# Kernel tuning notes

Measured on AMD Instinct MI355X. Metric: run time of the kernel, lower is better.

The kernel has to match this reference:

```python
import jax, jax.numpy as jnp
import numpy as np

N = 65536
NUM_STATE = 128
NUM_HIDDEN = 256
NUM_EMBED = 128


def setup_inputs() -> dict:
    key = jax.random.key(0)
    ks = jax.random.split(key, 8)
    s1 = jax.random.normal(ks[0], (N, NUM_STATE), dtype=jnp.float32)
    s2 = jax.random.normal(ks[1], (N, NUM_STATE), dtype=jnp.float32)
    # kaiming_normal_(fan_in, linear): std = 1/sqrt(fan_in)
    W1 = jax.random.normal(ks[2], (NUM_HIDDEN, NUM_STATE), dtype=jnp.float32) / np.sqrt(NUM_STATE)
    b1 = jnp.zeros((NUM_HIDDEN,), dtype=jnp.float32)
    W2 = jax.random.normal(ks[3], (NUM_HIDDEN, NUM_HIDDEN), dtype=jnp.float32) / np.sqrt(NUM_HIDDEN)
    b2 = jnp.zeros((NUM_HIDDEN,), dtype=jnp.float32)
    W3 = jax.random.normal(ks[4], (NUM_EMBED, NUM_HIDDEN), dtype=jnp.float32) / np.sqrt(NUM_HIDDEN)
    b3 = jnp.zeros((NUM_EMBED,), dtype=jnp.float32)
    return {"s1": s1, "s2": s2, "W1": W1, "b1": b1, "W2": W2, "b2": b2, "W3": W3, "b3": b3}


def _embed(x, W1, b1, W2, b2, W3, b3):
    h = jax.nn.selu(x @ W1.T + b1)
    h = jax.nn.selu(h @ W2.T + b2)
    return h @ W3.T + b3  # [N, num_embedding]


def reference(s1, s2, W1, b1, W2, b2, W3, b3):
    e1 = _embed(s1, W1, b1, W2, b2, W3, b3)
    e2 = _embed(s2, W1, b1, W2, b2, W3, b3)
    # diag(e1 @ e2.T) == per-row dot product (same math, O(N*d) not O(N^2*d))
    dots = jnp.einsum('nd,nd->n', e1, e2)
    out = dots / (jnp.linalg.norm(e1, axis=1) * jnp.linalg.norm(e2, axis=1))
    out = (out + 1.0) / 2.0
    return jax.nn.sigmoid(out)
```

## Files before the change

### kernel.cpp

```cpp
#include <hip/hip_runtime.h>


typedef __bf16 bf16x8 __attribute__((ext_vector_type(8)));
typedef __bf16 bf16x4 __attribute__((ext_vector_type(4)));
typedef float  f32x4  __attribute__((ext_vector_type(4)));

constexpr int WS_W1 = 0;
constexpr int WS_W2 = 32768;
constexpr int WS_W3 = 98304;

__device__ __forceinline__ float selu_f(float x) {
    const float scale = 1.0507009873554805f;
    const float sa    = 1.7580993408473766f;
    float xp = fmaxf(x, 0.f);
    float xn = fminf(x, 0.f);
    return fmaf(scale, xp, sa * (__expf(xn) - 1.f));
}

__device__ __forceinline__ bf16x8 read_act(const __bf16* lds, int row, int kcol) {
    unsigned byte = (unsigned)((row * 128 + kcol) * 2) ^ ((unsigned)(row & 7) << 4);
    return *(const bf16x8*)((const char*)lds + byte);
}

template<bool SELU>
__device__ __forceinline__ void store_act(__bf16* lds, int row, int col0, f32x4 a) {
    float v0 = a[0], v1 = a[1], v2 = a[2], v3 = a[3];
    if (SELU) { v0 = selu_f(v0); v1 = selu_f(v1); v2 = selu_f(v2); v3 = selu_f(v3); }
    bf16x4 u;
    u[0] = (__bf16)v0; u[1] = (__bf16)v1; u[2] = (__bf16)v2; u[3] = (__bf16)v3;
    unsigned byte = (unsigned)((row * 128 + col0) * 2) ^ ((unsigned)(row & 7) << 4);
    *(bf16x4*)((char*)lds + byte) = u;
}

__global__ void pack_weights_kernel(const float* __restrict__ W1,
                                    const float* __restrict__ W2,
                                    const float* __restrict__ W3,
                                    __bf16* __restrict__ ws) {
    int t = blockIdx.x * blockDim.x + threadIdx.x;
    const float* W; int K, KS, f, base;
    if (t < 4096)       { W = W1; K = 128; KS = 4; f = t;         base = WS_W1; }
    else if (t < 12288) { W = W2; K = 256; KS = 8; f = t - 4096;  base = WS_W2; }
    else                { W = W3; K = 256; KS = 8; f = t - 12288; base = WS_W3; }
    int lane = f & 63;
    int ks   = (f >> 6) % KS;
    int ct   = f / (64 * KS);
    int row  = ct * 16 + (lane & 15);
    int k0   = ks * 32 + (lane >> 4) * 8;
    const float* src = W + (size_t)row * K + k0;
    __bf16* dst = ws + base + (size_t)f * 8;
#pragma unroll
    for (int j = 0; j < 8; ++j) dst[j] = (__bf16)src[j];
}

__global__ __launch_bounds__(512, 4)
void embed_sim_kernel(const float* __restrict__ s1, const float* __restrict__ s2,
                      const float* __restrict__ b1, const float* __restrict__ b2,
                      const float* __restrict__ b3,
                      const __bf16* __restrict__ wf, float* __restrict__ out) {
    __shared__ __align__(16) __bf16 Xs[64 * 128];
    __shared__ __align__(16) __bf16 hA[64 * 128];
    __shared__ __align__(16) __bf16 hB[64 * 128];

    const int tid  = threadIdx.x;
    const int wave = tid >> 6;
    const int lane = tid & 63;
    const int lr   = lane & 15;
    const int kg   = lane >> 4;
    const int p0   = blockIdx.x * 32;

#pragma unroll
    for (int it = 0; it < 2; ++it) {
        int idx = tid + it * 512;
        int row = idx >> 4;
        int k0  = (idx & 15) << 3;
        const float* src = (row < 32) ? (s1 + (size_t)(p0 + row) * 128 + k0)
                                      : (s2 + (size_t)(p0 + row - 32) * 128 + k0);
        float4 v0 = *(const float4*)(src);
        float4 v1 = *(const float4*)(src + 4);
        bf16x8 w;
        w[0] = (__bf16)v0.x; w[1] = (__bf16)v0.y; w[2] = (__bf16)v0.z; w[3] = (__bf16)v0.w;
        w[4] = (__bf16)v1.x; w[5] = (__bf16)v1.y; w[6] = (__bf16)v1.z; w[7] = (__bf16)v1.w;
        unsigned byte = (unsigned)((row * 128 + k0) * 2) ^ ((unsigned)(row & 7) << 4);
        *(bf16x8*)((char*)Xs + byte) = w;
    }
    __syncthreads();

    {
        bf16x8 wfr[2][4]; f32x4 bv[2];
#pragma unroll
        for (int ti = 0; ti < 2; ++ti) {
            int t = wave * 2 + ti;
#pragma unroll
            for (int ks = 0; ks < 4; ++ks)
                wfr[ti][ks] = *(const bf16x8*)(wf + WS_W1 + (size_t)((t * 4 + ks) * 64 + lane) * 8);
            bv[ti] = *(const f32x4*)(b1 + t * 16 + kg * 4);
        }
#pragma unroll
        for (int s = 0; s < 4; ++s) {
            bf16x8 xfr[4];
#pragma unroll
            for (int ks = 0; ks < 4; ++ks) xfr[ks] = read_act(Xs, s * 16 + lr, ks * 32 + kg * 8);
#pragma unroll
            for (int ti = 0; ti < 2; ++ti) {
                f32x4 acc = bv[ti];
#pragma unroll
                for (int ks = 0; ks < 4; ++ks)
                    acc = __builtin_amdgcn_mfma_f32_16x16x32_bf16(wfr[ti][ks], xfr[ks], acc, 0, 0, 0);
                int t = wave * 2 + ti;
                store_act<true>((t < 8) ? hA : hB, s * 16 + lr, (t & 7) * 16 + kg * 4, acc);
            }
        }
    }
    __syncthreads();

    {
        f32x4 acc[2][4];
        bf16x8 wfr[2][8];
#pragma unroll
        for (int ti = 0; ti < 2; ++ti) {
            int t = wave * 2 + ti;
#pragma unroll
            for (int ks = 0; ks < 8; ++ks)
                wfr[ti][ks] = *(const bf16x8*)(wf + WS_W2 + (size_t)((t * 8 + ks) * 64 + lane) * 8);
            f32x4 b = *(const f32x4*)(b2 + t * 16 + kg * 4);
#pragma unroll
            for (int s = 0; s < 4; ++s) acc[ti][s] = b;
        }
#pragma unroll
        for (int s = 0; s < 4; ++s) {
            const int row = s * 16 + lr;
            bf16x8 hfr[8];
#pragma unroll
            for (int ks = 0; ks < 4; ++ks) {
                hfr[ks]     = read_act(hA, row, ks * 32 + kg * 8);
                hfr[4 + ks] = read_act(hB, row, ks * 32 + kg * 8);
            }
#pragma unroll
            for (int ti = 0; ti < 2; ++ti)
#pragma unroll
                for (int ks = 0; ks < 8; ++ks)
                    acc[ti][s] = __builtin_amdgcn_mfma_f32_16x16x32_bf16(
                        wfr[ti][ks], hfr[ks], acc[ti][s], 0, 0, 0);
        }
        if (wave < 4) {
#pragma unroll
            for (int ti = 0; ti < 2; ++ti)
#pragma unroll
                for (int s = 0; s < 4; ++s)
                    store_act<true>(Xs, s * 16 + lr, (wave * 2 + ti) * 16 + kg * 4, acc[ti][s]);
        }
        __syncthreads();
        if (wave >= 4) {
#pragma unroll
            for (int ti = 0; ti < 2; ++ti)
#pragma unroll
                for (int s = 0; s < 4; ++s)
                    store_act<true>(hA, s * 16 + lr, ((wave - 4) * 2 + ti) * 16 + kg * 4, acc[ti][s]);
        }
    }
    __syncthreads();

    {
        bf16x8 wfr[8]; f32x4 bv;
        const int t = wave;
#pragma unroll
        for (int ks = 0; ks < 8; ++ks)
            wfr[ks] = *(const bf16x8*)(wf + WS_W3 + (size_t)((t * 8 + ks) * 64 + lane) * 8);
        bv = *(const f32x4*)(b3 + t * 16 + kg * 4);
#pragma unroll
        for (int s = 0; s < 4; ++s) {
            const int row = s * 16 + lr;
            bf16x8 hfr[8];
#pragma unroll
            for (int ks = 0; ks < 4; ++ks) {
                hfr[ks]     = read_act(Xs, row, ks * 32 + kg * 8);
                hfr[4 + ks] = read_act(hA, row, ks * 32 + kg * 8);
            }
            f32x4 acc = bv;
#pragma unroll
            for (int ks = 0; ks < 8; ++ks)
                acc = __builtin_amdgcn_mfma_f32_16x16x32_bf16(wfr[ks], hfr[ks], acc, 0, 0, 0);
            store_act<false>(hB, row, t * 16 + kg * 4, acc);
        }
    }
    __syncthreads();

    const int p  = tid >> 4;
    const int dg = tid & 15;
    const int d0 = dg * 8;
    float dot = 0.f, n1 = 0.f, n2 = 0.f;
    {
        unsigned by1 = (unsigned)((p * 128 + d0) * 2) ^ ((unsigned)(p & 7) << 4);
        unsigned by2 = (unsigned)(((p + 32) * 128 + d0) * 2) ^ ((unsigned)((p + 32) & 7) << 4);
        bf16x8 e1 = *(const bf16x8*)((const char*)hB + by1);
        bf16x8 e2 = *(const bf16x8*)((const char*)hB + by2);
#pragma unroll
        for (int j = 0; j < 8; ++j) {
            float a = (float)e1[j], b = (float)e2[j];
            dot = fmaf(a, b, dot);
            n1  = fmaf(a, a, n1);
            n2  = fmaf(b, b, n2);
        }
    }
#pragma unroll
    for (int off = 1; off < 16; off <<= 1) {
        dot += __shfl_xor(dot, off);
        n1  += __shfl_xor(n1,  off);
        n2  += __shfl_xor(n2,  off);
    }
    if (dg == 0) {
        float r = dot * rsqrtf(n1 * n2);
        float x = (r + 1.f) * 0.5f;
        out[p0 + p] = 1.f / (1.f + __expf(-x));
    }
}

extern "C" void kernel_launch(void* const* d_in, const int* in_sizes, int n_in,
                              void* d_out, int out_size, void* d_ws, size_t ws_size,
                              hipStream_t stream) {
    const float* s1 = (const float*)d_in[0];
    const float* s2 = (const float*)d_in[1];
    const float* W1 = (const float*)d_in[2];
    const float* b1 = (const float*)d_in[3];
    const float* W2 = (const float*)d_in[4];
    const float* b2 = (const float*)d_in[5];
    const float* W3 = (const float*)d_in[6];
    const float* b3 = (const float*)d_in[7];
    __bf16* wf = (__bf16*)d_ws;
    float*  outp = (float*)d_out;

    pack_weights_kernel<<<64, 256, 0, stream>>>(W1, W2, W3, wf);

    const int npairs = in_sizes[0] / 128;
    embed_sim_kernel<<<npairs / 32, 512, 0, stream>>>(s1, s2, b1, b2, b3, wf, outp);
}
```

Measured before the change: 61.01 us.

## Halve block to 256 threads with more output tiles per wave

The fused embedding kernel now runs 4 waves per block instead of 8. Each wave computes twice as many output column tiles, and the layer-2 and layer-3 weights are loaded in two K halves to limit register pressure. The LDS layout moves from three 64x128 buffers to one 64x128 buffer plus one 64x256 buffer that is reused for the final embeddings. The aim is more MFMA work per wave and amortised activation fragment reads, in exchange for more accumulators per thread and changed occupancy limits (launch bounds 256,3).

After: 58.22 us. -4.6%, faster.

```diff
diff --git a/kernel.cpp b/kernel.cpp
--- a/kernel.cpp
+++ b/kernel.cpp
@@ -17,18 +17,19 @@
     return fmaf(scale, xp, sa * (__expf(xn) - 1.f));
 }
 
+template<int COLS>
 __device__ __forceinline__ bf16x8 read_act(const __bf16* lds, int row, int kcol) {
-    unsigned byte = (unsigned)((row * 128 + kcol) * 2) ^ ((unsigned)(row & 7) << 4);
+    unsigned byte = (unsigned)((row * COLS + kcol) * 2) ^ ((unsigned)(row & 7) << 4);
     return *(const bf16x8*)((const char*)lds + byte);
 }
 
-template<bool SELU>
+template<bool SELU, int COLS>
 __device__ __forceinline__ void store_act(__bf16* lds, int row, int col0, f32x4 a) {
     float v0 = a[0], v1 = a[1], v2 = a[2], v3 = a[3];
     if (SELU) { v0 = selu_f(v0); v1 = selu_f(v1); v2 = selu_f(v2); v3 = selu_f(v3); }
     bf16x4 u;
     u[0] = (__bf16)v0; u[1] = (__bf16)v1; u[2] = (__bf16)v2; u[3] = (__bf16)v3;
-    unsigned byte = (unsigned)((row * 128 + col0) * 2) ^ ((unsigned)(row & 7) << 4);
+    unsigned byte = (unsigned)((row * COLS + col0) * 2) ^ ((unsigned)(row & 7) << 4);
     *(bf16x4*)((char*)lds + byte) = u;
 }
 
@@ -52,14 +53,13 @@
     for (int j = 0; j < 8; ++j) dst[j] = (__bf16)src[j];
 }
 
-__global__ __launch_bounds__(512, 4)
+__global__ __launch_bounds__(256, 3)
 void embed_sim_kernel(const float* __restrict__ s1, const float* __restrict__ s2,
                       const float* __restrict__ b1, const float* __restrict__ b2,
                       const float* __restrict__ b3,
                       const __bf16* __restrict__ wf, float* __restrict__ out) {
     __shared__ __align__(16) __bf16 Xs[64 * 128];
-    __shared__ __align__(16) __bf16 hA[64 * 128];
-    __shared__ __align__(16) __bf16 hB[64 * 128];
+    __shared__ __align__(16) __bf16 hA[64 * 256];
 
     const int tid  = threadIdx.x;
     const int wave = tid >> 6;
@@ -68,9 +68,12 @@
     const int kg   = lane >> 4;
     const int p0   = blockIdx.x * 32;
 
-#pragma unroll
-    for (int it = 0; it < 2; ++it) {
-        int idx = tid + it * 512;
+    __bf16* h2hi = hA;
+    __bf16* Es   = hA + 64 * 128;
+
+#pragma unroll
+    for (int it = 0; it < 4; ++it) {
+        int idx = tid + it * 256;
         int row = idx >> 4;
         int k0  = (idx & 15) << 3;
         const float* src = (row < 32) ? (s1 + (size_t)(p0 + row) * 128 + k0)
@@ -86,10 +89,10 @@
     __syncthreads();
 
     {
-        bf16x8 wfr[2][4]; f32x4 bv[2];
-#pragma unroll
-        for (int ti = 0; ti < 2; ++ti) {
-            int t = wave * 2 + ti;
+        bf16x8 wfr[4][4]; f32x4 bv[4];
+#pragma unroll
+        for (int ti = 0; ti < 4; ++ti) {
+            int t = wave * 4 + ti;
 #pragma unroll
             for (int ks = 0; ks < 4; ++ks)
                 wfr[ti][ks] = *(const bf16x8*)(wf + WS_W1 + (size_t)((t * 4 + ks) * 64 + lane) * 8);
@@ -97,103 +100,125 @@
         }
 #pragma unroll
         for (int s = 0; s < 4; ++s) {
+            const int row = s * 16 + lr;
             bf16x8 xfr[4];
 #pragma unroll
-            for (int ks = 0; ks < 4; ++ks) xfr[ks] = read_act(Xs, s * 16 + lr, ks * 32 + kg * 8);
-#pragma unroll
-            for (int ti = 0; ti < 2; ++ti) {
+            for (int ks = 0; ks < 4; ++ks) xfr[ks] = read_act<128>(Xs, row, ks * 32 + kg * 8);
+#pragma unroll
+            for (int ti = 0; ti < 4; ++ti) {
                 f32x4 acc = bv[ti];
 #pragma unroll
                 for (int ks = 0; ks < 4; ++ks)
                     acc = __builtin_amdgcn_mfma_f32_16x16x32_bf16(wfr[ti][ks], xfr[ks], acc, 0, 0, 0);
-                int t = wave * 2 + ti;
-                store_act<true>((t < 8) ? hA : hB, s * 16 + lr, (t & 7) * 16 + kg * 4, acc);
-            }
+                store_act<true, 256>(hA, row, (wave * 4 + ti) * 16 + kg * 4, acc);
+            }
+        }
+    }
+    __syncthreads();
+
+    {
+        f32x4 acc[4][4];
+#pragma unroll
+        for (int ti = 0; ti < 4; ++ti) {
+            f32x4 b = *(const f32x4*)(b2 + (wave * 4 + ti) * 16 + kg * 4);
+#pragma unroll
+            for (int s = 0; s < 4; ++s) acc[ti][s] = b;
+        }
+#pragma unroll
+        for (int kh = 0; kh < 2; ++kh) {
+            bf16x8 wfr[4][4];
+#pragma unroll
+            for (int ti = 0; ti < 4; ++ti) {
+                int t = wave * 4 + ti;
+#pragma unroll
+                for (int ks = 0; ks < 4; ++ks)
+                    wfr[ti][ks] = *(const bf16x8*)(wf + WS_W2 + (size_t)((t * 8 + kh * 4 + ks) * 64 + lane) * 8);
+            }
+#pragma unroll
+            for (int s = 0; s < 4; ++s) {
+                const int row = s * 16 + lr;
+                bf16x8 hfr[4];
+#pragma unroll
+                for (int ks = 0; ks < 4; ++ks)
+                    hfr[ks] = read_act<256>(hA, row, kh * 128 + ks * 32 + kg * 8);
+#pragma unroll
+                for (int ti = 0; ti < 4; ++ti)
+#pragma unroll
+                    for (int ks = 0; ks < 4; ++ks)
+                        acc[ti][s] = __builtin_amdgcn_mfma_f32_16x16x32_bf16(
+                            wfr[ti][ks], hfr[ks], acc[ti][s], 0, 0, 0);
+            }
+        }
+        if (wave < 2) {
+#pragma unroll
+            for (int ti = 0; ti < 4; ++ti)
+#pragma unroll
+                for (int s = 0; s < 4; ++s)
+                    store_act<true, 128>(Xs, s * 16 + lr, (wave * 4 + ti) * 16 + kg * 4, acc[ti][s]);
+        }
+        __syncthreads();
+        if (wave >= 2) {
+#pragma unroll
+            for (int ti = 0; ti < 4; ++ti)
+#pragma unroll
+                for (int s = 0; s < 4; ++s)
+                    store_act<true, 128>(h2hi, s * 16 + lr, ((wave - 2) * 4 + ti) * 16 + kg * 4, acc[ti][s]);
         }
     }
     __syncthreads();
 
     {
         f32x4 acc[2][4];
-        bf16x8 wfr[2][8];
 #pragma unroll
         for (int ti = 0; ti < 2; ++ti) {
-            int t = wave * 2 + ti;
-#pragma unroll
-            for (int ks = 0; ks < 8; ++ks)
-                wfr[ti][ks] = *(const bf16x8*)(wf + WS_W2 + (size_t)((t * 8 + ks) * 64 + lane) * 8);
-            f32x4 b = *(const f32x4*)(b2 + t * 16 + kg * 4);
+            f32x4 b = *(const f32x4*)(b3 + (wave * 2 + ti) * 16 + kg * 4);
 #pragma unroll
             for (int s = 0; s < 4; ++s) acc[ti][s] = b;
         }
 #pragma unroll
-        for (int s = 0; s < 4; ++s) {
-            const int row = s * 16 + lr;
-            bf16x8 hfr[8];
-#pragma unroll
-            for (int ks = 0; ks < 4; ++ks) {
-                hfr[ks]     = read_act(hA, row, ks * 32 + kg * 8);
-                hfr[4 + ks] = read_act(hB, row, ks * 32 + kg * 8);
-            }
-#pragma unroll
-            for (int ti = 0; ti < 2; ++ti)
-#pragma unroll
-                for (int ks = 0; ks < 8; ++ks)
-                    acc[ti][s] = __builtin_amdgcn_mfma_f32_16x16x32_bf16(
-                        wfr[ti][ks], hfr[ks], acc[ti][s], 0, 0, 0);
-        }
-        if (wave < 4) {
-#pragma unroll
-            for (int ti = 0; ti < 2; ++ti)
-#pragma unroll
-                for (int s = 0; s < 4; ++s)
-                    store_act<true>(Xs, s * 16 + lr, (wave * 2 + ti) * 16 + kg * 4, acc[ti][s]);
-        }
-        __syncthreads();
-        if (wave >= 4) {
-#pragma unroll
-            for (int ti = 0; ti < 2; ++ti)
-#pragma unroll
-                for (int s = 0; s < 4; ++s)
-                    store_act<true>(hA, s * 16 + lr, ((wave - 4) * 2 + ti) * 16 + kg * 4, acc[ti][s]);
-        }
-    }
-    __syncthreads();
-
-    {
-        bf16x8 wfr[8]; f32x4 bv;
-        const int t = wave;
-#pragma unroll
-        for (int ks = 0; ks < 8; ++ks)
-            wfr[ks] = *(const bf16x8*)(wf + WS_W3 + (size_t)((t * 8 + ks) * 64 + lane) * 8);
-        bv = *(const f32x4*)(b3 + t * 16 + kg * 4);
-#pragma unroll
-        for (int s = 0; s < 4; ++s) {
-            const int row = s * 16 + lr;
-            bf16x8 hfr[8];
-#pragma unroll
-            for (int ks = 0; ks < 4; ++ks) {
-                hfr[ks]     = read_act(Xs, row, ks * 32 + kg * 8);
-                hfr[4 + ks] = read_act(hA, row, ks * 32 + kg * 8);
-            }
-            f32x4 acc = bv;
-#pragma unroll
-            for (int ks = 0; ks < 8; ++ks)
-                acc = __builtin_amdgcn_mfma_f32_16x16x32_bf16(wfr[ks], hfr[ks], acc, 0, 0, 0);
-            store_act<false>(hB, row, t * 16 + kg * 4, acc);
-        }
-    }
-    __syncthreads();
-
-    const int p  = tid >> 4;
-    const int dg = tid & 15;
-    const int d0 = dg * 8;
+        for (int kh = 0; kh < 2; ++kh) {
+            const __bf16* src = (kh == 0) ? Xs : h2hi;
+            bf16x8 wfr[2][4];
+#pragma unroll
+            for (int ti = 0; ti < 2; ++ti) {
+                int t = wave * 2 + ti;
+#pragma unroll
+                for (int ks = 0; ks < 4; ++ks)
+                    wfr[ti][ks] = *(const bf16x8*)(wf + WS_W3 + (size_t)((t * 8 + kh * 4 + ks) * 64 + lane) * 8);
+            }
+#pragma unroll
+            for (int s = 0; s < 4; ++s) {
+                const int row = s * 16 + lr;
+                bf16x8 hfr[4];
+#pragma unroll
+                for (int ks = 0; ks < 4; ++ks)
+                    hfr[ks] = read_act<128>(src, row, ks * 32 + kg * 8);
+#pragma unroll
+                for (int ti = 0; ti < 2; ++ti)
+#pragma unroll
+                    for (int ks = 0; ks < 4; ++ks)
+                        acc[ti][s] = __builtin_amdgcn_mfma_f32_16x16x32_bf16(
+                            wfr[ti][ks], hfr[ks], acc[ti][s], 0, 0, 0);
+            }
+        }
+#pragma unroll
+        for (int ti = 0; ti < 2; ++ti)
+#pragma unroll
+            for (int s = 0; s < 4; ++s)
+                store_act<false, 128>(Es, s * 16 + lr, (wave * 2 + ti) * 16 + kg * 4, acc[ti][s]);
+    }
+    __syncthreads();
+
+    const int p  = tid >> 3;
+    const int dg = tid & 7;
     float dot = 0.f, n1 = 0.f, n2 = 0.f;
-    {
+#pragma unroll
+    for (int half = 0; half < 2; ++half) {
+        int d0 = dg * 16 + half * 8;
         unsigned by1 = (unsigned)((p * 128 + d0) * 2) ^ ((unsigned)(p & 7) << 4);
         unsigned by2 = (unsigned)(((p + 32) * 128 + d0) * 2) ^ ((unsigned)((p + 32) & 7) << 4);
-        bf16x8 e1 = *(const bf16x8*)((const char*)hB + by1);
-        bf16x8 e2 = *(const bf16x8*)((const char*)hB + by2);
+        bf16x8 e1 = *(const bf16x8*)((const char*)Es + by1);
+        bf16x8 e2 = *(const bf16x8*)((const char*)Es + by2);
 #pragma unroll
         for (int j = 0; j < 8; ++j) {
             float a = (float)e1[j], b = (float)e2[j];
@@ -203,7 +228,7 @@
         }
     }
 #pragma unroll
-    for (int off = 1; off < 16; off <<= 1) {
+    for (int off = 1; off < 8; off <<= 1) {
         dot += __shfl_xor(dot, off);
         n1  += __shfl_xor(n1,  off);
         n2  += __shfl_xor(n2,  off);
@@ -232,5 +257,5 @@
     pack_weights_kernel<<<64, 256, 0, stream>>>(W1, W2, W3, wf);
 
     const int npairs = in_sizes[0] / 128;
-    embed_sim_kernel<<<npairs / 32, 512, 0, stream>>>(s1, s2, b1, b2, b3, wf, outp);
-}
+    embed_sim_kernel<<<npairs / 32, 256, 0, stream>>>(s1, s2, b1, b2, b3, wf, outp);
+}
```
